# Kernel tuning notes

Measured on AMD Instinct MI355X. Metric: run time of the kernel, lower is better.

Reference implementation:

```python
import jax, jax.numpy as jnp
import numpy as np

D_MODEL = 512
N_HEADS = 8
HEAD_DIM = D_MODEL // N_HEADS
D_FF = 2048
EPS = 1e-5


def layer_norm(x, gamma, beta):
    mu = jnp.mean(x, axis=-1, keepdims=True)
    var = jnp.mean((x - mu) ** 2, axis=-1, keepdims=True)
    return (x - mu) * jax.lax.rsqrt(var + EPS) * gamma + beta


def setup_inputs() -> dict:
    key = jax.random.key(0)
    ks = jax.random.split(key, 17)
    B, S = 2, 2048
    s_in = 1.0 / np.sqrt(D_MODEL)
    s_ff = 1.0 / np.sqrt(D_FF)
    return {
        "x": jax.random.normal(ks[0], (B, S, D_MODEL), jnp.float32),
        "Wq": jax.random.normal(ks[1], (D_MODEL, D_MODEL), jnp.float32) * s_in,
        "bq": jnp.zeros((D_MODEL,), jnp.float32),
        "Wk": jax.random.normal(ks[2], (D_MODEL, D_MODEL), jnp.float32) * s_in,
        "bk": jnp.zeros((D_MODEL,), jnp.float32),
        "Wv": jax.random.normal(ks[3], (D_MODEL, D_MODEL), jnp.float32) * s_in,
        "bv": jnp.zeros((D_MODEL,), jnp.float32),
        "Wo": jax.random.normal(ks[4], (D_MODEL, D_MODEL), jnp.float32) * s_in,
        "bo": jnp.zeros((D_MODEL,), jnp.float32),
        "W1": jax.random.normal(ks[5], (D_MODEL, D_FF), jnp.float32) * s_in,
        "b1": jnp.zeros((D_FF,), jnp.float32),
        "W2": jax.random.normal(ks[6], (D_FF, D_MODEL), jnp.float32) * s_ff,
        "b2": jnp.zeros((D_MODEL,), jnp.float32),
        "g1": jnp.ones((D_MODEL,), jnp.float32),
        "be1": jnp.zeros((D_MODEL,), jnp.float32),
        "g2": jnp.ones((D_MODEL,), jnp.float32),
        "be2": jnp.zeros((D_MODEL,), jnp.float32),
    }


def reference(x, Wq, bq, Wk, bk, Wv, bv, Wo, bo, W1, b1, W2, b2, g1, be1, g2, be2):
    B, S, _ = x.shape
    # projections + split heads -> [B, H, S, Dh]
    def heads(t):
        return t.reshape(B, S, N_HEADS, HEAD_DIM).transpose(0, 2, 1, 3)
    q = heads(x @ Wq + bq)
    k = heads(x @ Wk + bk)
    v = heads(x @ Wv + bv)
    # explicit scaled dot-product attention (full [B,H,S,S] scores as in source)
    scores = jnp.einsum('bhqd,bhkd->bhqk', q, k) / np.sqrt(HEAD_DIM).astype(np.float32)
    attn = jax.nn.softmax(scores, axis=-1)
    ctx = jnp.einsum('bhqk,bhkd->bhqd', attn, v)
    ctx = ctx.transpose(0, 2, 1, 3).reshape(B, S, D_MODEL)
    attn_out = ctx @ Wo + bo
    # post-norm residual 1
    h = layer_norm(x + attn_out, g1, be1)
    # FFN
    ff = jax.nn.relu(h @ W1 + b1) @ W2 + b2
    # post-norm residual 2
    return layer_norm(h + ff, g2, be2)
```

## Files before the change

### kernel.cpp

```cpp
#include <hip/hip_runtime.h>
#include <cmath>

#define D_MODEL 512
#define N_HEADS 8
#define HEAD_DIM 64
#define D_FF 2048
#define SEQ 2048
#define BATCH 2
#define MROWS (BATCH * SEQ)

typedef __attribute__((ext_vector_type(8))) short short8;
typedef __attribute__((ext_vector_type(4))) float float4v;
typedef unsigned short ushort_t;

static __device__ __forceinline__ ushort_t f2bf(float f) {
    union { float f; unsigned u; } v; v.f = f;
    unsigned r = (v.u + 0x7FFFu + ((v.u >> 16) & 1u)) >> 16;
    return (ushort_t)r;
}
static __device__ __forceinline__ ushort_t f2bf_trunc(float f) {
    union { float f; unsigned u; } v; v.f = f;
    return (ushort_t)(v.u >> 16);
}

static __device__ __forceinline__ void gload16(const void* g, void* l) {
    __builtin_amdgcn_global_load_lds(
        (__attribute__((address_space(1))) void*)(unsigned long long)g,
        (__attribute__((address_space(3))) void*)(unsigned)(unsigned long long)l,
        16, 0, 0);
}

__global__ __launch_bounds__(256) void prep_k(
    const float* __restrict__ x,
    const float* __restrict__ Wq, const float* __restrict__ Wk,
    const float* __restrict__ Wv, const float* __restrict__ Wo,
    const float* __restrict__ W1, const float* __restrict__ W2,
    ushort_t* __restrict__ xb,
    ushort_t* __restrict__ WqkvT, ushort_t* __restrict__ WoT,
    ushort_t* __restrict__ W1T, ushort_t* __restrict__ W2T)
{
    int tile = blockIdx.x;
    if (tile >= 3072) {
        int i = (tile - 3072) * 256 + threadIdx.x;
        float4 f = ((const float4*)x)[i];
        ushort4 o;
        o.x = f2bf(f.x); o.y = f2bf(f.y); o.z = f2bf(f.z); o.w = f2bf(f.w);
        ((ushort4*)xb)[i] = o;
        return;
    }
    const float* src; ushort_t* dst; int Kd, Nd, tloc;
    if (tile < 1024) {
        int wsel = tile >> 8; tloc = tile & 255; Kd = 512; Nd = 512;
        if (wsel == 0)      { src = Wq; dst = WqkvT; }
        else if (wsel == 1) { src = Wk; dst = WqkvT + (size_t)512 * 512; }
        else if (wsel == 2) { src = Wv; dst = WqkvT + (size_t)1024 * 512; }
        else                { src = Wo; dst = WoT; }
    } else if (tile < 2048) { tloc = tile - 1024; Kd = 512;  Nd = 2048; src = W1; dst = W1T; }
    else                    { tloc = tile - 2048; Kd = 2048; Nd = 512;  src = W2; dst = W2T; }
    int tn = Nd >> 5;
    int k0 = (tloc / tn) << 5, n0 = (tloc % tn) << 5;
    __shared__ float tl[32][33];
    int c = threadIdx.x & 31, r = threadIdx.x >> 5;
    #pragma unroll
    for (int i = 0; i < 4; ++i)
        tl[r + i * 8][c] = src[(size_t)(k0 + r + i * 8) * Nd + n0 + c];
    __syncthreads();
    #pragma unroll
    for (int i = 0; i < 4; ++i)
        dst[(size_t)(n0 + r + i * 8) * Kd + k0 + c] = f2bf(tl[c][r + i * 8]);
}

template <int MODE>
__global__ __launch_bounds__(256) void gemm_std_k(
    const ushort_t* __restrict__ A, const ushort_t* __restrict__ BT,
    const float* __restrict__ bias, void* __restrict__ Cv,
    int N, int K, int Klen, size_t zstride)
{
    __shared__ ushort_t As[64 * 128];
    __shared__ ushort_t Bs[128 * 128];

    const int t = threadIdx.x;
    const int w = t >> 6, lane = t & 63, l16 = lane & 15, quad = lane >> 4;
    const int m0 = blockIdx.y * 64;
    const int n0 = blockIdx.x * 128;
    const int kbase = blockIdx.z * Klen;
    const int mbase = (w >> 1) * 32;
    const int nbase = (w & 1) * 64;
    const int lrow = lane >> 4;
    const int lchunk = lane & 15;

    float4v acc[2][4];
    #pragma unroll
    for (int mt = 0; mt < 2; ++mt)
        #pragma unroll
        for (int nt = 0; nt < 4; ++nt)
            acc[mt][nt] = (float4v){0.f, 0.f, 0.f, 0.f};

    for (int ks = kbase; ks < kbase + Klen; ks += 128) {
        __syncthreads();
        for (int c = w; c < 16; c += 4) {
            int rl = c * 4 + lrow;
            gload16(A + (size_t)(m0 + rl) * K + ks + ((lchunk ^ (rl & 7)) << 3),
                    &As[c * 512]);
        }
        for (int c = w; c < 32; c += 4) {
            int rl = c * 4 + lrow;
            gload16(BT + (size_t)(n0 + rl) * K + ks + ((lchunk ^ (rl & 7)) << 3),
                    &Bs[c * 512]);
        }
        __syncthreads();

        #pragma unroll
        for (int co = 0; co < 4; ++co) {
            const int poff = (((co * 4 + quad) ^ (l16 & 7)) << 3);
            short8 af[2], bf8[4];
            #pragma unroll
            for (int mt = 0; mt < 2; ++mt)
                af[mt] = *(const short8*)&As[(mbase + mt * 16 + l16) * 128 + poff];
            #pragma unroll
            for (int nt = 0; nt < 4; ++nt)
                bf8[nt] = *(const short8*)&Bs[(nbase + nt * 16 + l16) * 128 + poff];
            #pragma unroll
            for (int mt = 0; mt < 2; ++mt)
                #pragma unroll
                for (int nt = 0; nt < 4; ++nt)
                    acc[mt][nt] = __builtin_amdgcn_mfma_f32_16x16x32_bf16(
                        af[mt], bf8[nt], acc[mt][nt], 0, 0, 0);
        }
    }

    float* Cf = (float*)Cv + blockIdx.z * zstride;
    #pragma unroll
    for (int mt = 0; mt < 2; ++mt) {
        #pragma unroll
        for (int nt = 0; nt < 4; ++nt) {
            int gcol = n0 + nbase + nt * 16 + l16;
            float b = (MODE == 2) ? 0.f : bias[gcol];
            #pragma unroll
            for (int r = 0; r < 4; ++r) {
                int grow = m0 + mbase + mt * 16 + quad * 4 + r;
                float v = acc[mt][nt][r] + b;
                if (MODE == 1) v = fmaxf(v, 0.f);
                if (MODE == 1) ((ushort_t*)Cv)[(size_t)grow * N + gcol] = f2bf(v);
                else           Cf[(size_t)grow * N + gcol] = v;
            }
        }
    }
}

__global__ __launch_bounds__(256) void gemm_qkv_k(
    const ushort_t* __restrict__ A, const ushort_t* __restrict__ BT,
    const float* __restrict__ bq, const float* __restrict__ bk,
    const float* __restrict__ bv,
    ushort_t* __restrict__ Qb, ushort_t* __restrict__ Kb,
    ushort_t* __restrict__ VTb)
{
    __shared__ ushort_t As[64 * 128];
    __shared__ ushort_t Bs[128 * 128];

    const int t = threadIdx.x;
    const int w = t >> 6, lane = t & 63, l16 = lane & 15, quad = lane >> 4;
    const int m0 = blockIdx.y * 64;
    const int n0 = blockIdx.x * 128;
    const int mbase = (w >> 1) * 32;
    const int nbase = (w & 1) * 64;
    const int lrow = lane >> 4;
    const int lchunk = lane & 15;
    const int K = 512;

    float4v acc[2][4];
    #pragma unroll
    for (int mt = 0; mt < 2; ++mt)
        #pragma unroll
        for (int nt = 0; nt < 4; ++nt)
            acc[mt][nt] = (float4v){0.f, 0.f, 0.f, 0.f};

    for (int ks = 0; ks < 512; ks += 128) {
        __syncthreads();
        for (int c = w; c < 16; c += 4) {
            int rl = c * 4 + lrow;
            gload16(A + (size_t)(m0 + rl) * K + ks + ((lchunk ^ (rl & 7)) << 3),
                    &As[c * 512]);
        }
        for (int c = w; c < 32; c += 4) {
            int rl = c * 4 + lrow;
            gload16(BT + (size_t)(n0 + rl) * K + ks + ((lchunk ^ (rl & 7)) << 3),
                    &Bs[c * 512]);
        }
        __syncthreads();

        #pragma unroll
        for (int co = 0; co < 4; ++co) {
            const int poff = (((co * 4 + quad) ^ (l16 & 7)) << 3);
            short8 af[2], bf8[4];
            #pragma unroll
            for (int mt = 0; mt < 2; ++mt)
                af[mt] = *(const short8*)&As[(mbase + mt * 16 + l16) * 128 + poff];
            #pragma unroll
            for (int nt = 0; nt < 4; ++nt)
                bf8[nt] = *(const short8*)&Bs[(nbase + nt * 16 + l16) * 128 + poff];
            #pragma unroll
            for (int mt = 0; mt < 2; ++mt)
                #pragma unroll
                for (int nt = 0; nt < 4; ++nt)
                    acc[mt][nt] = __builtin_amdgcn_mfma_f32_16x16x32_bf16(
                        af[mt], bf8[nt], acc[mt][nt], 0, 0, 0);
        }
    }

    const int tsel = n0 >> 9;
    const float* bias = (tsel == 0) ? bq : (tsel == 1) ? bk : bv;
    const float scl = (tsel == 0) ? 0.18033688f : 1.0f;
    ushort_t* dst = (tsel == 0) ? Qb : Kb;

    #pragma unroll
    for (int mt = 0; mt < 2; ++mt) {
        #pragma unroll
        for (int nt = 0; nt < 4; ++nt) {
            int gcol = n0 + nbase + nt * 16 + l16;
            int lcol = gcol - (tsel << 9);
            int h = lcol >> 6, dh = lcol & 63;
            float b = bias[lcol];
            #pragma unroll
            for (int r = 0; r < 4; ++r) {
                int grow = m0 + mbase + mt * 16 + quad * 4 + r;
                int bb = grow >> 11, s = grow & 2047;
                float v = (acc[mt][nt][r] + b) * scl;
                if (tsel < 2)
                    dst[(((size_t)(bb * N_HEADS + h)) * SEQ + s) * HEAD_DIM + dh] = f2bf(v);
                else
                    VTb[(((size_t)(bb * N_HEADS + h)) * HEAD_DIM + dh) * SEQ + s] = f2bf(v);
            }
        }
    }
}

__global__ __launch_bounds__(256) void attn_mfma_k(
    const ushort_t* __restrict__ Qg, const ushort_t* __restrict__ Kg,
    const ushort_t* __restrict__ VTg,
    float* __restrict__ Opart, float* __restrict__ Lpart)
{
    __shared__ __align__(16) ushort_t Ks[64 * 72];
    __shared__ __align__(16) ushort_t Vs[64 * 72];
    __shared__ __align__(16) ushort_t Ps[4][16 * 64];

    const int bh = blockIdx.x;
    const int q0 = blockIdx.y * 64;
    const int ks = blockIdx.z;
    const int t = threadIdx.x;
    const int w = t >> 6;
    const int lane = t & 63;
    const int l16 = lane & 15;
    const int quad = lane >> 4;
    const int qbase = q0 + w * 16;
    const float M2 = 14.4269504f;

    short8 aq[2];
    {
        const ushort_t* qp = Qg + ((size_t)bh * SEQ + qbase + l16) * HEAD_DIM + quad * 8;
        aq[0] = *(const short8*)(qp);
        aq[1] = *(const short8*)(qp + 32);
    }

    float4v o[4] = {};
    float l_acc[4] = {0.f, 0.f, 0.f, 0.f};

    for (int kt = 0; kt < 16; ++kt) {
        const int kbase = ks * 1024 + kt * 64;
        __syncthreads();
        #pragma unroll
        for (int lit = 0; lit < 2; ++lit) {
            int flat = lit * 256 + t;
            int row = flat >> 3;
            int c0 = (flat & 7) * 8;
            *(short8*)&Ks[row * 72 + c0] =
                *(const short8*)(Kg + ((size_t)bh * SEQ + kbase + row) * HEAD_DIM + c0);
            *(short8*)&Vs[row * 72 + c0] =
                *(const short8*)(VTg + ((size_t)bh * HEAD_DIM + row) * SEQ + kbase + c0);
        }
        __syncthreads();

        float4v s[4];
        #pragma unroll
        for (int nt = 0; nt < 4; ++nt) s[nt] = (float4v){0.f, 0.f, 0.f, 0.f};
        #pragma unroll
        for (int c = 0; c < 2; ++c) {
            #pragma unroll
            for (int nt = 0; nt < 4; ++nt) {
                short8 bk8 = *(const short8*)&Ks[(nt * 16 + l16) * 72 + c * 32 + quad * 8];
                s[nt] = __builtin_amdgcn_mfma_f32_16x16x32_bf16(aq[c], bk8, s[nt], 0, 0, 0);
            }
        }

        #pragma unroll
        for (int nt = 0; nt < 4; ++nt) {
            #pragma unroll
            for (int r = 0; r < 4; ++r) {
                float p = exp2f(s[nt][r] - M2);
                s[nt][r] = p;
                l_acc[r] += p;
            }
        }

        #pragma unroll
        for (int nt = 0; nt < 4; ++nt)
            #pragma unroll
            for (int r = 0; r < 4; ++r) {
                int row = quad * 4 + r;
                int key = nt * 16 + l16;
                Ps[w][row * 64 + (((key >> 3) ^ (row & 7)) << 3) + (key & 7)] =
                    f2bf_trunc(s[nt][r]);
            }
        asm volatile("s_waitcnt lgkmcnt(0)" ::: "memory");

        #pragma unroll
        for (int c = 0; c < 2; ++c) {
            short8 ap = *(const short8*)&Ps[w][l16 * 64 + ((((c << 2) + quad) ^ (l16 & 7)) << 3)];
            #pragma unroll
            for (int dt = 0; dt < 4; ++dt) {
                short8 bv8 = *(const short8*)&Vs[(dt * 16 + l16) * 72 + c * 32 + quad * 8];
                o[dt] = __builtin_amdgcn_mfma_f32_16x16x32_bf16(ap, bv8, o[dt], 0, 0, 0);
            }
        }
    }

    const size_t pbase = ((size_t)(ks * 16 + bh)) * SEQ;
    #pragma unroll
    for (int r = 0; r < 4; ++r) {
        float L = l_acc[r];
        #pragma unroll
        for (int msk = 1; msk < 16; msk <<= 1) L += __shfl_xor(L, msk);
        int qrow = qbase + quad * 4 + r;
        if (l16 == 0) Lpart[pbase + qrow] = L;
        #pragma unroll
        for (int dt = 0; dt < 4; ++dt)
            Opart[(pbase + qrow) * HEAD_DIM + dt * 16 + l16] = o[dt][r];
    }
}

__global__ __launch_bounds__(256) void attn_comb_k(
    const float* __restrict__ Op, const float* __restrict__ Lp,
    ushort_t* __restrict__ ctx)
{
    int g = blockIdx.x * 256 + threadIdx.x;
    int d4 = g & 15;
    int q  = (g >> 4) & 2047;
    int bh = g >> 15;
    float ax = 0.f, ay = 0.f, az = 0.f, aw = 0.f, L = 0.f;
    #pragma unroll
    for (int ks = 0; ks < 2; ++ks) {
        size_t row = ((size_t)(ks * 16 + bh) * SEQ + q) * HEAD_DIM;
        float4 a = ((const float4*)(Op + row))[d4];
        ax += a.x; ay += a.y; az += a.z; aw += a.w;
        L += Lp[ks * 16 * SEQ + bh * SEQ + q];
    }
    float inv = 1.0f / L;
    ushort4 o4;
    o4.x = f2bf(ax * inv);
    o4.y = f2bf(ay * inv);
    o4.z = f2bf(az * inv);
    o4.w = f2bf(aw * inv);
    int bb = bh >> 3, hh = bh & 7;
    *(ushort4*)&ctx[((size_t)(bb * SEQ + q)) * D_MODEL + hh * HEAD_DIM + d4 * 4] = o4;
}

template <int WRITE_BF>
__global__ __launch_bounds__(256) void add_ln_k(
    const float* __restrict__ X, const float* __restrict__ P0,
    const float* __restrict__ P1, const float* __restrict__ bias,
    const float* __restrict__ gam, const float* __restrict__ bet,
    float* __restrict__ O, ushort_t* __restrict__ Ob)
{
    const int row = blockIdx.x;
    const int t = threadIdx.x;
    const size_t ro = (size_t)row * D_MODEL;

    float v0 = X[ro + t]       + P0[ro + t]       + P1[ro + t]       + bias[t];
    float v1 = X[ro + t + 256] + P0[ro + t + 256] + P1[ro + t + 256] + bias[t + 256];
    float s = v0 + v1;
    float ss = v0 * v0 + v1 * v1;
    #pragma unroll
    for (int off = 32; off > 0; off >>= 1) {
        s  += __shfl_down(s, off);
        ss += __shfl_down(ss, off);
    }
    __shared__ float sb[4], ssb[4];
    if ((t & 63) == 0) { sb[t >> 6] = s; ssb[t >> 6] = ss; }
    __syncthreads();
    float S  = sb[0] + sb[1] + sb[2] + sb[3];
    float SS = ssb[0] + ssb[1] + ssb[2] + ssb[3];
    float mu  = S * (1.0f / D_MODEL);
    float var = SS * (1.0f / D_MODEL) - mu * mu;
    float inv = rsqrtf(var + 1e-5f);
    float o0 = (v0 - mu) * inv * gam[t] + bet[t];
    float o1 = (v1 - mu) * inv * gam[t + 256] + bet[t + 256];
    O[ro + t]       = o0;
    O[ro + t + 256] = o1;
    if (WRITE_BF) {
        Ob[ro + t]       = f2bf(o0);
        Ob[ro + t + 256] = f2bf(o1);
    }
}

extern "C" void kernel_launch(void* const* d_in, const int* in_sizes, int n_in,
                              void* d_out, int out_size, void* d_ws, size_t ws_size,
                              hipStream_t stream)
{
    const float* x   = (const float*)d_in[0];
    const float* Wq  = (const float*)d_in[1];
    const float* bq  = (const float*)d_in[2];
    const float* Wk  = (const float*)d_in[3];
    const float* bk  = (const float*)d_in[4];
    const float* Wv  = (const float*)d_in[5];
    const float* bv  = (const float*)d_in[6];
    const float* Wo  = (const float*)d_in[7];
    const float* bo  = (const float*)d_in[8];
    const float* W1  = (const float*)d_in[9];
    const float* b1  = (const float*)d_in[10];
    const float* W2  = (const float*)d_in[11];
    const float* b2  = (const float*)d_in[12];
    const float* g1  = (const float*)d_in[13];
    const float* be1 = (const float*)d_in[14];
    const float* g2  = (const float*)d_in[15];
    const float* be2 = (const float*)d_in[16];
    float* out = (float*)d_out;
    float* ws  = (float*)d_ws;

    ushort_t* WoT   = (ushort_t*)(ws);
    ushort_t* W1T   = (ushort_t*)(ws + 131072);
    ushort_t* W2T   = (ushort_t*)(ws + 655360);
    ushort_t* WqkvT = (ushort_t*)(ws + 1179648);
    ushort_t* xb    = (ushort_t*)(ws + 1572864);
    ushort_t* Qb    = (ushort_t*)(ws + 2621440);
    ushort_t* Kb    = (ushort_t*)(ws + 3670016);
    ushort_t* VTb   = (ushort_t*)(ws + 4718592);
    ushort_t* Ctx   = (ushort_t*)(ws + 5767168);
    float*    Lpart = ws + 6815744;
    float*    Hh    = ws + 6881280;
    float*    P0    = ws + 8978432;
    float*    P1    = ws + 11075584;
    float*    Opart = ws + 8978432;
    ushort_t* FF1   = (ushort_t*)(ws + 1572864);
    ushort_t* Hhb   = (ushort_t*)(ws + 5767168);

    prep_k<<<5120, 256, 0, stream>>>(x, Wq, Wk, Wv, Wo, W1, W2, xb, WqkvT, WoT, W1T, W2T);

    gemm_qkv_k<<<dim3(12, 64), 256, 0, stream>>>(xb, WqkvT, bq, bk, bv, Qb, Kb, VTb);

    attn_mfma_k<<<dim3(16, 32, 2), 256, 0, stream>>>(Qb, Kb, VTb, Opart, Lpart);
    attn_comb_k<<<2048, 256, 0, stream>>>(Opart, Lpart, Ctx);

    gemm_std_k<2><<<dim3(4, 64, 2), 256, 0, stream>>>(
        Ctx, WoT, nullptr, P0, 512, 512, 256, (size_t)MROWS * D_MODEL);

    add_ln_k<1><<<4096, 256, 0, stream>>>(x, P0, P1, bo, g1, be1, Hh, Hhb);

    gemm_std_k<1><<<dim3(16, 64), 256, 0, stream>>>(
        Hhb, W1T, b1, FF1, 2048, 512, 512, 0);

    gemm_std_k<2><<<dim3(4, 64, 2), 256, 0, stream>>>(
        FF1, W2T, nullptr, P0, 512, 2048, 1024, (size_t)MROWS * D_MODEL);

    add_ln_k<0><<<4096, 256, 0, stream>>>(Hh, P0, P1, b2, g2, be2, out, (ushort_t*)nullptr);
}
```

Measured before the change: 226.6 us.

## Double-buffer K/V tiles in attention with async global-to-LDS loads and XOR swizzle

Result: faster. 221.1 us (-2.5%).

```diff
diff --git a/kernel.cpp b/kernel.cpp
--- a/kernel.cpp
+++ b/kernel.cpp
@@ -240,8 +240,8 @@
     const ushort_t* __restrict__ VTg,
     float* __restrict__ Opart, float* __restrict__ Lpart)
 {
-    __shared__ __align__(16) ushort_t Ks[64 * 72];
-    __shared__ __align__(16) ushort_t Vs[64 * 72];
+    __shared__ __align__(16) ushort_t Kbuf[2][64 * 64];
+    __shared__ __align__(16) ushort_t Vbuf[2][64 * 64];
     __shared__ __align__(16) ushort_t Ps[4][16 * 64];
 
     const int bh = blockIdx.x;
@@ -255,6 +255,21 @@
     const int qbase = q0 + w * 16;
     const float M2 = 14.4269504f;
 
+    const int r0 = t >> 3;
+    const int r1 = r0 + 32;
+    const int g0 = (t & 7) ^ (r0 & 7);
+    const int g1 = (t & 7) ^ (r1 & 7);
+    const size_t kgrow = (size_t)bh * SEQ;
+    const size_t vgrow = (size_t)bh * HEAD_DIM;
+
+#define ATTN_STAGE(b, kb)                                                       \
+    {                                                                           \
+        gload16(Kg + (kgrow + (kb) + r0) * HEAD_DIM + g0 * 8, &Kbuf[b][w * 512]);          \
+        gload16(Kg + (kgrow + (kb) + r1) * HEAD_DIM + g1 * 8, &Kbuf[b][2048 + w * 512]);   \
+        gload16(VTg + (vgrow + r0) * SEQ + (kb) + g0 * 8, &Vbuf[b][w * 512]);              \
+        gload16(VTg + (vgrow + r1) * SEQ + (kb) + g1 * 8, &Vbuf[b][2048 + w * 512]);       \
+    }
+
     short8 aq[2];
     {
         const ushort_t* qp = Qg + ((size_t)bh * SEQ + qbase + l16) * HEAD_DIM + quad * 8;
@@ -265,29 +280,30 @@
     float4v o[4] = {};
     float l_acc[4] = {0.f, 0.f, 0.f, 0.f};
 
+    ATTN_STAGE(0, ks * 1024)
+
     for (int kt = 0; kt < 16; ++kt) {
-        const int kbase = ks * 1024 + kt * 64;
-        __syncthreads();
-        #pragma unroll
-        for (int lit = 0; lit < 2; ++lit) {
-            int flat = lit * 256 + t;
-            int row = flat >> 3;
-            int c0 = (flat & 7) * 8;
-            *(short8*)&Ks[row * 72 + c0] =
-                *(const short8*)(Kg + ((size_t)bh * SEQ + kbase + row) * HEAD_DIM + c0);
-            *(short8*)&Vs[row * 72 + c0] =
-                *(const short8*)(VTg + ((size_t)bh * HEAD_DIM + row) * SEQ + kbase + c0);
-        }
-        __syncthreads();
+        const int cur = kt & 1;
+        if (kt < 15) {
+            ATTN_STAGE(cur ^ 1, ks * 1024 + (kt + 1) * 64)
+            asm volatile("s_waitcnt vmcnt(4)" ::: "memory");
+        } else {
+            asm volatile("s_waitcnt vmcnt(0)" ::: "memory");
+        }
+        asm volatile("s_barrier" ::: "memory");
+
+        const ushort_t* Kc = Kbuf[cur];
+        const ushort_t* Vc = Vbuf[cur];
 
         float4v s[4];
         #pragma unroll
         for (int nt = 0; nt < 4; ++nt) s[nt] = (float4v){0.f, 0.f, 0.f, 0.f};
         #pragma unroll
         for (int c = 0; c < 2; ++c) {
+            const int poff = (((c * 4 + quad) ^ (l16 & 7)) << 3);
             #pragma unroll
             for (int nt = 0; nt < 4; ++nt) {
-                short8 bk8 = *(const short8*)&Ks[(nt * 16 + l16) * 72 + c * 32 + quad * 8];
+                short8 bk8 = *(const short8*)&Kc[(nt * 16 + l16) * 64 + poff];
                 s[nt] = __builtin_amdgcn_mfma_f32_16x16x32_bf16(aq[c], bk8, s[nt], 0, 0, 0);
             }
         }
@@ -316,13 +332,17 @@
         #pragma unroll
         for (int c = 0; c < 2; ++c) {
             short8 ap = *(const short8*)&Ps[w][l16 * 64 + ((((c << 2) + quad) ^ (l16 & 7)) << 3)];
+            const int poff = (((c * 4 + quad) ^ (l16 & 7)) << 3);
             #pragma unroll
             for (int dt = 0; dt < 4; ++dt) {
-                short8 bv8 = *(const short8*)&Vs[(dt * 16 + l16) * 72 + c * 32 + quad * 8];
+                short8 bv8 = *(const short8*)&Vc[(dt * 16 + l16) * 64 + poff];
                 o[dt] = __builtin_amdgcn_mfma_f32_16x16x32_bf16(ap, bv8, o[dt], 0, 0, 0);
             }
         }
-    }
+
+        asm volatile("s_barrier" ::: "memory");
+    }
+#undef ATTN_STAGE
 
     const size_t pbase = ((size_t)(ks * 16 + bh)) * SEQ;
     #pragma unroll
```
